# Kernel tuning notes

Hardware: AMD Instinct MI355X
Metric: run time of the kernel (lower is better)

## Reference

```python
import jax, jax.numpy as jnp
import numpy as np

N = 50000      # num_nodes
E = 800000     # num_edges (avg degree 16)
D = 128        # embedding_dim
HID = 32       # per-head hidden dim of conv1
H = 8          # heads of conv1
OUT = 128      # output_dim


def setup_inputs() -> dict:
    key = jax.random.key(0)
    ks = jax.random.split(key, 14)
    s = lambda fan_in: 1.0 / np.sqrt(fan_in)
    return {
        "x": jax.random.randint(ks[0], (N,), 0, N),
        "edge_index": jax.random.randint(ks[1], (2, E), 0, N),
        "emb": jax.random.normal(ks[2], (N, D), jnp.float32),
        # conv1: GATConv(D, HID, heads=H, concat=True)
        "W1": jax.random.normal(ks[3], (D, H * HID), jnp.float32) * s(D),
        "a_src1": jax.random.normal(ks[4], (H, HID), jnp.float32) * s(HID),
        "a_dst1": jax.random.normal(ks[5], (H, HID), jnp.float32) * s(HID),
        "b1": jnp.zeros((H * HID,), jnp.float32),
        # conv2: GATConv(H*HID, OUT, heads=1, concat=False)
        "W2": jax.random.normal(ks[6], (H * HID, OUT), jnp.float32) * s(H * HID),
        "a_src2": jax.random.normal(ks[7], (1, OUT), jnp.float32) * s(OUT),
        "a_dst2": jax.random.normal(ks[8], (1, OUT), jnp.float32) * s(OUT),
        "b2": jnp.zeros((OUT,), jnp.float32),
        # output Linear(OUT, OUT)
        "Wo": jax.random.normal(ks[9], (OUT, OUT), jnp.float32) * s(OUT),
        "bo": jnp.zeros((OUT,), jnp.float32),
    }


def _segment_softmax(e, seg, n):
    # e: [E, H]; softmax over edges sharing the same destination node
    m = jax.ops.segment_max(e, seg, num_segments=n)            # [N, H]
    ex = jnp.exp(e - m[seg])
    denom = jax.ops.segment_sum(ex, seg, num_segments=n)       # [N, H]
    return ex / (denom[seg] + 1e-16)


def _gat_conv(x, src, dst, W, a_src, a_dst, b, concat):
    n = x.shape[0]
    Hh, C = a_src.shape
    h = (x @ W).reshape(n, Hh, C)                              # [N, H, C]
    al_src = (h * a_src).sum(-1)                               # [N, H]
    al_dst = (h * a_dst).sum(-1)                               # [N, H]
    e = jax.nn.leaky_relu(al_src[src] + al_dst[dst], 0.2)      # [E, H]
    alpha = _segment_softmax(e, dst, n)                        # [E, H]
    out = jax.ops.segment_sum(h[src] * alpha[:, :, None], dst, num_segments=n)
    out = out.reshape(n, Hh * C) if concat else out.mean(axis=1)
    return out + b


def reference(x, edge_index, emb, W1, a_src1, a_dst1, b1,
              W2, a_src2, a_dst2, b2, Wo, bo):
    n = x.shape[0]
    loops = jnp.arange(n)
    src = jnp.concatenate([edge_index[0], loops])              # add self-loops (PyG default)
    dst = jnp.concatenate([edge_index[1], loops])
    h = emb[x]                                                 # [N, D]
    h = _gat_conv(h, src, dst, W1, a_src1, a_dst1, b1, concat=True)
    h = _gat_conv(h, src, dst, W2, a_src2, a_dst2, b2, concat=False)
    return h @ Wo + bo
```

## Files before the change

kernel.cpp:

```cpp
#include <hip/hip_runtime.h>
#include <hip/hip_bf16.h>

#define NN 50000
#define EE 800000
#define DD 128
#define F1 256
#define F2 128

using short8  = __attribute__((ext_vector_type(8))) short;
using floatx4 = __attribute__((ext_vector_type(4))) float;

__device__ inline float bf2f(ushort u) { return __uint_as_float(((unsigned)u) << 16); }
__device__ inline ushort f2bf(float f) {
    unsigned u = __float_as_uint(f);
    u += 0x7fffu + ((u >> 16) & 1u);
    return (ushort)(u >> 16);
}

#define HB ((EE + 255) / 256)
#define GB ((NN + 1) / 2)
#define W1B ((DD * F1 + 255) / 256)
#define W2B ((F1 * F2 + 255) / 256)

__global__ __launch_bounds__(256) void k_prep(
    const int* __restrict__ edst, int* __restrict__ cnt,
    const int* __restrict__ x, const float* __restrict__ emb, ushort* __restrict__ Ax,
    const float* __restrict__ W1, ushort* __restrict__ W1t,
    const float* __restrict__ W2, ushort* __restrict__ W2t,
    const float* __restrict__ Wo, ushort* __restrict__ Wot) {
    int b = blockIdx.x;
    if (b < HB) {
        int i = b * 256 + threadIdx.x;
        if (i < EE) atomicAdd(&cnt[edst[i]], 1);
    } else if (b < HB + GB) {
        int row = (b - HB) * 2 + (threadIdx.x >> 7);
        if (row < NN) {
            int c = threadIdx.x & 127;
            Ax[(size_t)row * DD + c] = f2bf(emb[(size_t)x[row] * DD + c]);
        }
    } else if (b < HB + GB + W1B) {
        int idx = (b - HB - GB) * 256 + threadIdx.x;
        int k = idx / F1, n = idx % F1;
        W1t[(size_t)n * DD + k] = f2bf(W1[(size_t)k * F1 + n]);
    } else if (b < HB + GB + W1B + W2B) {
        int idx = (b - HB - GB - W1B) * 256 + threadIdx.x;
        int k = idx / F2, n = idx % F2;
        W2t[(size_t)n * F1 + k] = f2bf(W2[(size_t)k * F2 + n]);
    } else {
        int idx = (b - HB - GB - W1B - W2B) * 256 + threadIdx.x;
        int k = idx / F2, n = idx % F2;
        Wot[(size_t)n * F2 + k] = f2bf(Wo[(size_t)k * F2 + n]);
    }
}

__global__ void k_scan1(const int* __restrict__ cnt, int* __restrict__ out,
                        int* __restrict__ sums) {
    __shared__ int s[256];
    int i = blockIdx.x * 256 + threadIdx.x;
    int v = (i < NN) ? cnt[i] + 1 : 0;
    s[threadIdx.x] = v;
    __syncthreads();
    for (int off = 1; off < 256; off <<= 1) {
        int t = (threadIdx.x >= off) ? s[threadIdx.x - off] : 0;
        __syncthreads();
        s[threadIdx.x] += t;
        __syncthreads();
    }
    if (i < NN) out[i] = s[threadIdx.x] - v;
    if (threadIdx.x == 255) sums[blockIdx.x] = s[255];
}

__global__ void k_scan2(int* __restrict__ sums, int nb) {
    __shared__ int s[256];
    int v = (threadIdx.x < nb) ? sums[threadIdx.x] : 0;
    s[threadIdx.x] = v;
    __syncthreads();
    for (int off = 1; off < 256; off <<= 1) {
        int t = (threadIdx.x >= off) ? s[threadIdx.x - off] : 0;
        __syncthreads();
        s[threadIdx.x] += t;
        __syncthreads();
    }
    if (threadIdx.x < nb) sums[threadIdx.x] = s[threadIdx.x] - v;
}

__global__ void k_scan3(int* __restrict__ offsets, const int* __restrict__ sums,
                        int* __restrict__ cursor) {
    int i = blockIdx.x * 256 + threadIdx.x;
    if (i < NN) {
        int v = offsets[i] + sums[blockIdx.x];
        offsets[i] = v;
        cursor[i] = v;
    }
    if (blockIdx.x == 0 && threadIdx.x == 0) offsets[NN] = EE + NN;
}

__global__ void k_scatter(const int* __restrict__ esrc, const int* __restrict__ edst,
                          int* __restrict__ cursor, int* __restrict__ srcs) {
    int i = blockIdx.x * 256 + threadIdx.x;
    if (i < EE) {
        int pos = atomicAdd(&cursor[edst[i]], 1);
        srcs[pos] = esrc[i];
    } else if (i < EE + NN) {
        int n = i - EE;
        int pos = atomicAdd(&cursor[n], 1);
        srcs[pos] = n;
    }
}

template<int K, bool FINAL>
__global__ __launch_bounds__(256, 2) void k_mfma_gemm(
    const ushort* __restrict__ A, const ushort* __restrict__ Bt,
    void* __restrict__ Cout, int ldc, const float* __restrict__ bias) {
    __shared__ ushort As[128][72];
    __shared__ ushort Bs[128][72];
    const int t    = threadIdx.x;
    const int lane = t & 63;
    const int w    = t >> 6;
    const int wr   = w >> 1, wc = w & 1;
    const int m0   = blockIdx.x * 128;
    const int n0   = blockIdx.y * 128;
    floatx4 acc[4][4] = {};
    for (int k0 = 0; k0 < K; k0 += 64) {
        #pragma unroll
        for (int p = 0; p < 4; ++p) {
            int linear = p * 2048 + t * 8;
            int row = linear >> 6;
            int col = linear & 63;
            short8 va = {};
            int gm = m0 + row;
            if (gm < NN) va = *(const short8*)(A + (size_t)gm * K + k0 + col);
            *(short8*)&As[row][col] = va;
            short8 vb = *(const short8*)(Bt + (size_t)(n0 + row) * K + k0 + col);
            *(short8*)&Bs[row][col] = vb;
        }
        __syncthreads();
        #pragma unroll
        for (int kk = 0; kk < 64; kk += 32) {
            const int q8 = (lane >> 4) * 8;
            short8 af[4], bf[4];
            #pragma unroll
            for (int i = 0; i < 4; ++i)
                af[i] = *(const short8*)&As[wr * 64 + i * 16 + (lane & 15)][kk + q8];
            #pragma unroll
            for (int j = 0; j < 4; ++j)
                bf[j] = *(const short8*)&Bs[wc * 64 + j * 16 + (lane & 15)][kk + q8];
            #pragma unroll
            for (int i = 0; i < 4; ++i)
                #pragma unroll
                for (int j = 0; j < 4; ++j)
                    acc[i][j] = __builtin_amdgcn_mfma_f32_16x16x32_bf16(
                        af[i], bf[j], acc[i][j], 0, 0, 0);
        }
        __syncthreads();
    }
    const int r0 = (lane >> 4) * 4;
    const int cc = lane & 15;
    #pragma unroll
    for (int i = 0; i < 4; ++i) {
        #pragma unroll
        for (int r = 0; r < 4; ++r) {
            int m = m0 + wr * 64 + i * 16 + r0 + r;
            if (m >= NN) continue;
            #pragma unroll
            for (int j = 0; j < 4; ++j) {
                int n = n0 + wc * 64 + j * 16 + cc;
                float v = acc[i][j][r];
                if (FINAL) ((float*)Cout)[(size_t)m * ldc + n] = v + bias[n];
                else       ((ushort*)Cout)[(size_t)m * ldc + n] = f2bf(v);
            }
        }
    }
}

__global__ __launch_bounds__(256) void k_al1(const ushort* __restrict__ h1,
                                             const float* __restrict__ a_src1,
                                             const float* __restrict__ a_dst1,
                                             float* __restrict__ a1s, float* __restrict__ a1d) {
    int n = blockIdx.x * 4 + (threadIdx.x >> 6);
    if (n >= NN) return;
    int lane = threadIdx.x & 63;
    ushort4 hu = *(const ushort4*)(h1 + (size_t)n * F1 + lane * 4);
    float4 hv = make_float4(bf2f(hu.x), bf2f(hu.y), bf2f(hu.z), bf2f(hu.w));
    float4 as  = *(const float4*)(a_src1 + lane * 4);
    float4 adv = *(const float4*)(a_dst1 + lane * 4);
    float ps = hv.x * as.x + hv.y * as.y + hv.z * as.z + hv.w * as.w;
    float pd = hv.x * adv.x + hv.y * adv.y + hv.z * adv.z + hv.w * adv.w;
    #pragma unroll
    for (int off = 1; off < 8; off <<= 1) {
        ps += __shfl_xor(ps, off);
        pd += __shfl_xor(pd, off);
    }
    if ((lane & 7) == 0) {
        a1s[n * 8 + (lane >> 3)] = ps;
        a1d[n * 8 + (lane >> 3)] = pd;
    }
}

__global__ __launch_bounds__(256) void k_al2(const ushort* __restrict__ h2,
                                             const float* __restrict__ a_src2,
                                             const float* __restrict__ a_dst2,
                                             float* __restrict__ a2s, float* __restrict__ a2d) {
    int n = blockIdx.x * 4 + (threadIdx.x >> 6);
    if (n >= NN) return;
    int lane = threadIdx.x & 63;
    ushort2 hu = *(const ushort2*)(h2 + (size_t)n * F2 + lane * 2);
    float2 hv = make_float2(bf2f(hu.x), bf2f(hu.y));
    float2 as  = *(const float2*)(a_src2 + lane * 2);
    float2 adv = *(const float2*)(a_dst2 + lane * 2);
    float ps = hv.x * as.x + hv.y * as.y;
    float pd = hv.x * adv.x + hv.y * adv.y;
    #pragma unroll
    for (int off = 1; off < 64; off <<= 1) {
        ps += __shfl_xor(ps, off);
        pd += __shfl_xor(pd, off);
    }
    if (lane == 0) { a2s[n] = ps; a2d[n] = pd; }
}

__device__ inline float lrelu(float x) { return x > 0.f ? x : 0.2f * x; }

__global__ __launch_bounds__(256) void k_agg1(
    const int* __restrict__ offsets, const int* __restrict__ srcs,
    const ushort* __restrict__ h1, const float* __restrict__ a1s,
    const float* __restrict__ a1d, const float* __restrict__ b1,
    ushort* __restrict__ out1) {
    __shared__ float atab[4][512];
    __shared__ int   stab[4][64];
    const int w = threadIdx.x >> 6;
    const int d = blockIdx.x * 4 + w;
    if (d >= NN) return;
    const int lane = threadIdx.x & 63;
    const int beg = offsets[d], end = offsets[d + 1];
    const int e8 = lane >> 3, h8 = lane & 7;
    const float ad = a1d[d * 8 + h8];
    float m = -1e30f, den = 0.f;
    for (int i = beg + e8; i < end; i += 8) {
        int s = srcs[i];
        float v = lrelu(a1s[s * 8 + h8] + ad);
        float nm = fmaxf(m, v);
        den = den * __expf(m - nm) + __expf(v - nm);
        m = nm;
    }
    #pragma unroll
    for (int mask = 8; mask < 64; mask <<= 1) {
        float om = __shfl_xor(m, mask);
        float od = __shfl_xor(den, mask);
        float nm = fmaxf(m, om);
        den = den * __expf(m - nm) + od * __expf(om - nm);
        m = nm;
    }
    float rden = 1.f / (den + 1e-16f);
    const int sl = ((lane & 7) << 3) | (lane >> 3);
    const float mh  = __shfl(m, sl);
    const float rdh = __shfl(rden, sl);
    float4 acc = make_float4(0.f, 0.f, 0.f, 0.f);
    const int hh = lane >> 3;
    for (int tb = beg; tb < end; tb += 64) {
        int cnt = min(64, end - tb);
        if (lane < cnt) stab[w][lane] = srcs[tb + lane];
        int np = cnt * 8;
        for (int p = lane; p < np; p += 64) {
            int s = stab[w][p >> 3];
            float v = lrelu(a1s[s * 8 + h8] + ad);
            atab[w][p] = __expf(v - m) * rden;
        }
        for (int e = 0; e < cnt; ++e) {
            int s = stab[w][e];
            float alpha = atab[w][e * 8 + hh];
            ushort4 u = *(const ushort4*)(h1 + (size_t)s * F1 + lane * 4);
            acc.x += alpha * bf2f(u.x); acc.y += alpha * bf2f(u.y);
            acc.z += alpha * bf2f(u.z); acc.w += alpha * bf2f(u.w);
        }
    }
    (void)mh; (void)rdh;
    float4 bb = *(const float4*)(b1 + lane * 4);
    ushort4 o;
    o.x = f2bf(acc.x + bb.x); o.y = f2bf(acc.y + bb.y);
    o.z = f2bf(acc.z + bb.z); o.w = f2bf(acc.w + bb.w);
    *(ushort4*)(out1 + (size_t)d * F1 + lane * 4) = o;
}

__global__ __launch_bounds__(256) void k_agg2(
    const int* __restrict__ offsets, const int* __restrict__ srcs,
    const ushort* __restrict__ h2, const float* __restrict__ a2s,
    const float* __restrict__ a2d, const float* __restrict__ b2,
    ushort* __restrict__ out2) {
    __shared__ float atab[4][64];
    __shared__ int   stab[4][64];
    const int w = threadIdx.x >> 6;
    const int d = blockIdx.x * 4 + w;
    if (d >= NN) return;
    const int lane = threadIdx.x & 63;
    const int beg = offsets[d], end = offsets[d + 1];
    const float ad = a2d[d];
    float m = -1e30f, den = 0.f;
    for (int i = beg + lane; i < end; i += 64) {
        int s = srcs[i];
        float v = lrelu(a2s[s] + ad);
        float nm = fmaxf(m, v);
        den = den * __expf(m - nm) + __expf(v - nm);
        m = nm;
    }
    #pragma unroll
    for (int mask = 1; mask < 64; mask <<= 1) {
        float om = __shfl_xor(m, mask);
        float od = __shfl_xor(den, mask);
        float nm = fmaxf(m, om);
        den = den * __expf(m - nm) + od * __expf(om - nm);
        m = nm;
    }
    float rden = 1.f / (den + 1e-16f);
    float2 acc = make_float2(0.f, 0.f);
    for (int tb = beg; tb < end; tb += 64) {
        int cnt = min(64, end - tb);
        if (lane < cnt) {
            int s = srcs[tb + lane];
            stab[w][lane] = s;
            atab[w][lane] = __expf(lrelu(a2s[s] + ad) - m) * rden;
        }
        for (int e = 0; e < cnt; ++e) {
            int s = stab[w][e];
            float alpha = atab[w][e];
            ushort2 u = *(const ushort2*)(h2 + (size_t)s * F2 + lane * 2);
            acc.x += alpha * bf2f(u.x); acc.y += alpha * bf2f(u.y);
        }
    }
    float2 bb = *(const float2*)(b2 + lane * 2);
    ushort2 o;
    o.x = f2bf(acc.x + bb.x); o.y = f2bf(acc.y + bb.y);
    *(ushort2*)(out2 + (size_t)d * F2 + lane * 2) = o;
}

extern "C" void kernel_launch(void* const* d_in, const int* in_sizes, int n_in,
                              void* d_out, int out_size, void* d_ws, size_t ws_size,
                              hipStream_t stream) {
    const int*   x      = (const int*)d_in[0];
    const int*   edge   = (const int*)d_in[1];
    const float* emb    = (const float*)d_in[2];
    const float* W1     = (const float*)d_in[3];
    const float* a_src1 = (const float*)d_in[4];
    const float* a_dst1 = (const float*)d_in[5];
    const float* b1     = (const float*)d_in[6];
    const float* W2     = (const float*)d_in[7];
    const float* a_src2 = (const float*)d_in[8];
    const float* a_dst2 = (const float*)d_in[9];
    const float* b2     = (const float*)d_in[10];
    const float* Wo     = (const float*)d_in[11];
    const float* bo     = (const float*)d_in[12];
    float* out = (float*)d_out;

    char* w = (char*)d_ws;
    auto alloc = [&](size_t bytes) {
        char* p = w;
        w += (bytes + 255) & ~(size_t)255;
        return p;
    };
    int*    offsets = (int*)alloc((NN + 1) * sizeof(int));
    int*    cursor  = (int*)alloc(NN * sizeof(int));
    int*    sums    = (int*)alloc(256 * sizeof(int));
    int*    srcs    = (int*)alloc((size_t)(EE + NN) * sizeof(int));
    ushort* Ax      = (ushort*)alloc((size_t)NN * DD * sizeof(ushort));
    ushort* W1t     = (ushort*)alloc((size_t)DD * F1 * sizeof(ushort));
    ushort* W2t     = (ushort*)alloc((size_t)F1 * F2 * sizeof(ushort));
    ushort* Wot     = (ushort*)alloc((size_t)F2 * F2 * sizeof(ushort));
    ushort* h1      = (ushort*)alloc((size_t)NN * F1 * sizeof(ushort));
    ushort* out1    = (ushort*)alloc((size_t)NN * F1 * sizeof(ushort));
    ushort* h2      = (ushort*)alloc((size_t)NN * F2 * sizeof(ushort));
    ushort* out2    = (ushort*)alloc((size_t)NN * F2 * sizeof(ushort));
    float*  a1s     = (float*)alloc((size_t)NN * 8 * sizeof(float));
    float*  a1d     = (float*)alloc((size_t)NN * 8 * sizeof(float));
    float*  a2s     = a1s;
    float*  a2d     = a1d;

    const int* esrc = edge;
    const int* edst = edge + EE;

    const int NB = (NN + 255) / 256;

    hipMemsetAsync(cursor, 0, NN * sizeof(int), stream);
    k_prep<<<HB + GB + W1B + W2B + ((F2 * F2 + 255) / 256), 256, 0, stream>>>(
        edst, cursor, x, emb, Ax, W1, W1t, W2, W2t, Wo, Wot);
    k_scan1<<<NB, 256, 0, stream>>>(cursor, offsets, sums);
    k_scan2<<<1, 256, 0, stream>>>(sums, NB);
    k_scan3<<<NB, 256, 0, stream>>>(offsets, sums, cursor);
    k_scatter<<<(EE + NN + 255) / 256, 256, 0, stream>>>(esrc, edst, cursor, srcs);

    const int MT = (NN + 127) / 128;

    k_mfma_gemm<DD, false><<<dim3(MT, F1 / 128), 256, 0, stream>>>(Ax, W1t, h1, F1, nullptr);
    k_al1<<<(NN + 3) / 4, 256, 0, stream>>>(h1, a_src1, a_dst1, a1s, a1d);
    k_agg1<<<(NN + 3) / 4, 256, 0, stream>>>(offsets, srcs, h1, a1s, a1d, b1, out1);

    k_mfma_gemm<F1, false><<<dim3(MT, 1), 256, 0, stream>>>(out1, W2t, h2, F2, nullptr);
    k_al2<<<(NN + 3) / 4, 256, 0, stream>>>(h2, a_src2, a_dst2, a2s, a2d);
    k_agg2<<<(NN + 3) / 4, 256, 0, stream>>>(offsets, srcs, h2, a2s, a2d, b2, out2);

    k_mfma_gemm<F2, true><<<dim3(MT, 1), 256, 0, stream>>>(out2, Wot, out, F2, bo);
}
```

Before: 378.4 us.

## Fuse attention logits into GEMM epilogues, merge scan kernels, unroll gather loops

Computes the per-head source and destination attention logits inside the MFMA GEMM epilogue from fp32 accumulators, using cross-lane shuffles and shared memory. This removes the separate k_al1 and k_al2 kernels that re-read h1 and h2 from memory. It also folds the single-block scan of block sums into the offset-add kernel, so every block redundantly rescans the sums, and unrolls the aggregation gather loops by four to put more loads in flight. The logits now come from unrounded fp32 values rather than the bf16-rounded h, which slightly changes numerics, and the epilogue adds shuffle and register work.

```diff
diff --git a/kernel.cpp b/kernel.cpp
--- a/kernel.cpp
+++ b/kernel.cpp
@@ -21,6 +21,7 @@
 #define GB ((NN + 1) / 2)
 #define W1B ((DD * F1 + 255) / 256)
 #define W2B ((F1 * F2 + 255) / 256)
+#define WOB ((F2 * F2 + 255) / 256)
 
 __global__ __launch_bounds__(256) void k_prep(
     const int* __restrict__ edst, int* __restrict__ cnt,
@@ -70,7 +71,8 @@
     if (threadIdx.x == 255) sums[blockIdx.x] = s[255];
 }
 
-__global__ void k_scan2(int* __restrict__ sums, int nb) {
+__global__ void k_scan3(int* __restrict__ offsets, const int* __restrict__ sums,
+                        int* __restrict__ cursor, int nb) {
     __shared__ int s[256];
     int v = (threadIdx.x < nb) ? sums[threadIdx.x] : 0;
     s[threadIdx.x] = v;
@@ -81,16 +83,12 @@
         s[threadIdx.x] += t;
         __syncthreads();
     }
-    if (threadIdx.x < nb) sums[threadIdx.x] = s[threadIdx.x] - v;
-}
-
-__global__ void k_scan3(int* __restrict__ offsets, const int* __restrict__ sums,
-                        int* __restrict__ cursor) {
+    int base = (blockIdx.x == 0) ? 0 : s[blockIdx.x - 1];
     int i = blockIdx.x * 256 + threadIdx.x;
     if (i < NN) {
-        int v = offsets[i] + sums[blockIdx.x];
-        offsets[i] = v;
-        cursor[i] = v;
+        int o = offsets[i] + base;
+        offsets[i] = o;
+        cursor[i] = o;
     }
     if (blockIdx.x == 0 && threadIdx.x == 0) offsets[NN] = EE + NN;
 }
@@ -108,12 +106,15 @@
     }
 }
 
-template<int K, bool FINAL>
+template<int K, int MODE>
 __global__ __launch_bounds__(256, 2) void k_mfma_gemm(
     const ushort* __restrict__ A, const ushort* __restrict__ Bt,
-    void* __restrict__ Cout, int ldc, const float* __restrict__ bias) {
+    void* __restrict__ Cout, int ldc, const float* __restrict__ bias,
+    const float* __restrict__ avs, const float* __restrict__ avd,
+    float* __restrict__ out_s, float* __restrict__ out_d) {
     __shared__ ushort As[128][72];
     __shared__ ushort Bs[128][72];
+    __shared__ float als[2][128], ald[2][128];
     const int t    = threadIdx.x;
     const int lane = t & 63;
     const int w    = t >> 6;
@@ -154,68 +155,76 @@
         }
         __syncthreads();
     }
-    const int r0 = (lane >> 4) * 4;
+    const int q  = lane >> 4;
+    const int r0 = q * 4;
     const int cc = lane & 15;
+    float as0, as1, as2, as3, ad0, ad1, ad2, ad3;
+    if (MODE == 1 || MODE == 2) {
+        as0 = avs[n0 + wc * 64 +  0 + cc]; ad0 = avd[n0 + wc * 64 +  0 + cc];
+        as1 = avs[n0 + wc * 64 + 16 + cc]; ad1 = avd[n0 + wc * 64 + 16 + cc];
+        as2 = avs[n0 + wc * 64 + 32 + cc]; ad2 = avd[n0 + wc * 64 + 32 + cc];
+        as3 = avs[n0 + wc * 64 + 48 + cc]; ad3 = avd[n0 + wc * 64 + 48 + cc];
+    }
     #pragma unroll
     for (int i = 0; i < 4; ++i) {
         #pragma unroll
         for (int r = 0; r < 4; ++r) {
             int m = m0 + wr * 64 + i * 16 + r0 + r;
-            if (m >= NN) continue;
-            #pragma unroll
-            for (int j = 0; j < 4; ++j) {
-                int n = n0 + wc * 64 + j * 16 + cc;
-                float v = acc[i][j][r];
-                if (FINAL) ((float*)Cout)[(size_t)m * ldc + n] = v + bias[n];
-                else       ((ushort*)Cout)[(size_t)m * ldc + n] = f2bf(v);
+            if (MODE == 1) {
+                float hs0 = acc[i][0][r] * as0 + acc[i][1][r] * as1;
+                float hs1 = acc[i][2][r] * as2 + acc[i][3][r] * as3;
+                float hd0 = acc[i][0][r] * ad0 + acc[i][1][r] * ad1;
+                float hd1 = acc[i][2][r] * ad2 + acc[i][3][r] * ad3;
+                #pragma unroll
+                for (int mask = 1; mask < 16; mask <<= 1) {
+                    hs0 += __shfl_xor(hs0, mask);
+                    hs1 += __shfl_xor(hs1, mask);
+                    hd0 += __shfl_xor(hd0, mask);
+                    hd1 += __shfl_xor(hd1, mask);
+                }
+                if (cc == 0 && m < NN) {
+                    int gh = (n0 >> 5) + wc * 2;
+                    out_s[m * 8 + gh] = hs0;   out_s[m * 8 + gh + 1] = hs1;
+                    out_d[m * 8 + gh] = hd0;   out_d[m * 8 + gh + 1] = hd1;
+                }
             }
-        }
-    }
-}
-
-__global__ __launch_bounds__(256) void k_al1(const ushort* __restrict__ h1,
-                                             const float* __restrict__ a_src1,
-                                             const float* __restrict__ a_dst1,
-                                             float* __restrict__ a1s, float* __restrict__ a1d) {
-    int n = blockIdx.x * 4 + (threadIdx.x >> 6);
-    if (n >= NN) return;
-    int lane = threadIdx.x & 63;
-    ushort4 hu = *(const ushort4*)(h1 + (size_t)n * F1 + lane * 4);
-    float4 hv = make_float4(bf2f(hu.x), bf2f(hu.y), bf2f(hu.z), bf2f(hu.w));
-    float4 as  = *(const float4*)(a_src1 + lane * 4);
-    float4 adv = *(const float4*)(a_dst1 + lane * 4);
-    float ps = hv.x * as.x + hv.y * as.y + hv.z * as.z + hv.w * as.w;
-    float pd = hv.x * adv.x + hv.y * adv.y + hv.z * adv.z + hv.w * adv.w;
-    #pragma unroll
-    for (int off = 1; off < 8; off <<= 1) {
-        ps += __shfl_xor(ps, off);
-        pd += __shfl_xor(pd, off);
-    }
-    if ((lane & 7) == 0) {
-        a1s[n * 8 + (lane >> 3)] = ps;
-        a1d[n * 8 + (lane >> 3)] = pd;
-    }
-}
-
-__global__ __launch_bounds__(256) void k_al2(const ushort* __restrict__ h2,
-                                             const float* __restrict__ a_src2,
-                                             const float* __restrict__ a_dst2,
-                                             float* __restrict__ a2s, float* __restrict__ a2d) {
-    int n = blockIdx.x * 4 + (threadIdx.x >> 6);
-    if (n >= NN) return;
-    int lane = threadIdx.x & 63;
-    ushort2 hu = *(const ushort2*)(h2 + (size_t)n * F2 + lane * 2);
-    float2 hv = make_float2(bf2f(hu.x), bf2f(hu.y));
-    float2 as  = *(const float2*)(a_src2 + lane * 2);
-    float2 adv = *(const float2*)(a_dst2 + lane * 2);
-    float ps = hv.x * as.x + hv.y * as.y;
-    float pd = hv.x * adv.x + hv.y * adv.y;
-    #pragma unroll
-    for (int off = 1; off < 64; off <<= 1) {
-        ps += __shfl_xor(ps, off);
-        pd += __shfl_xor(pd, off);
-    }
-    if (lane == 0) { a2s[n] = ps; a2d[n] = pd; }
+            if (MODE == 2) {
+                float ps = acc[i][0][r] * as0 + acc[i][1][r] * as1
+                         + acc[i][2][r] * as2 + acc[i][3][r] * as3;
+                float pd = acc[i][0][r] * ad0 + acc[i][1][r] * ad1
+                         + acc[i][2][r] * ad2 + acc[i][3][r] * ad3;
+                #pragma unroll
+                for (int mask = 1; mask < 16; mask <<= 1) {
+                    ps += __shfl_xor(ps, mask);
+                    pd += __shfl_xor(pd, mask);
+                }
+                if (cc == 0) {
+                    int lr = wr * 64 + i * 16 + r0 + r;
+                    als[wc][lr] = ps;
+                    ald[wc][lr] = pd;
+                }
+            }
+            if (m < NN) {
+                #pragma unroll
+                for (int j = 0; j < 4; ++j) {
+                    int n = n0 + wc * 64 + j * 16 + cc;
+                    float v = acc[i][j][r];
+                    if (MODE == 3) ((float*)Cout)[(size_t)m * ldc + n] = v + bias[n];
+                    else           ((ushort*)Cout)[(size_t)m * ldc + n] = f2bf(v);
+                }
+            }
+        }
+    }
+    if (MODE == 2) {
+        __syncthreads();
+        if (t < 128) {
+            int m = m0 + t;
+            if (m < NN) {
+                out_s[m] = als[0][t] + als[1][t];
+                out_d[m] = ald[0][t] + ald[1][t];
+            }
+        }
+    }
 }
 
 __device__ inline float lrelu(float x) { return x > 0.f ? x : 0.2f * x; }
@@ -251,9 +260,6 @@
         m = nm;
     }
     float rden = 1.f / (den + 1e-16f);
-    const int sl = ((lane & 7) << 3) | (lane >> 3);
-    const float mh  = __shfl(m, sl);
-    const float rdh = __shfl(rden, sl);
     float4 acc = make_float4(0.f, 0.f, 0.f, 0.f);
     const int hh = lane >> 3;
     for (int tb = beg; tb < end; tb += 64) {
@@ -265,7 +271,24 @@
             float v = lrelu(a1s[s * 8 + h8] + ad);
             atab[w][p] = __expf(v - m) * rden;
         }
-        for (int e = 0; e < cnt; ++e) {
+        int e = 0;
+        for (; e + 4 <= cnt; e += 4) {
+            int s0 = stab[w][e], s1 = stab[w][e + 1];
+            int s2 = stab[w][e + 2], s3 = stab[w][e + 3];
+            ushort4 u0 = *(const ushort4*)(h1 + (size_t)s0 * F1 + lane * 4);
+            ushort4 u1 = *(const ushort4*)(h1 + (size_t)s1 * F1 + lane * 4);
+            ushort4 u2 = *(const ushort4*)(h1 + (size_t)s2 * F1 + lane * 4);
+            ushort4 u3 = *(const ushort4*)(h1 + (size_t)s3 * F1 + lane * 4);
+            float a0 = atab[w][(e + 0) * 8 + hh];
+            float a1 = atab[w][(e + 1) * 8 + hh];
+            float a2 = atab[w][(e + 2) * 8 + hh];
+            float a3 = atab[w][(e + 3) * 8 + hh];
+            acc.x += a0 * bf2f(u0.x) + a1 * bf2f(u1.x) + a2 * bf2f(u2.x) + a3 * bf2f(u3.x);
+            acc.y += a0 * bf2f(u0.y) + a1 * bf2f(u1.y) + a2 * bf2f(u2.y) + a3 * bf2f(u3.y);
+            acc.z += a0 * bf2f(u0.z) + a1 * bf2f(u1.z) + a2 * bf2f(u2.z) + a3 * bf2f(u3.z);
+            acc.w += a0 * bf2f(u0.w) + a1 * bf2f(u1.w) + a2 * bf2f(u2.w) + a3 * bf2f(u3.w);
+        }
+        for (; e < cnt; ++e) {
             int s = stab[w][e];
             float alpha = atab[w][e * 8 + hh];
             ushort4 u = *(const ushort4*)(h1 + (size_t)s * F1 + lane * 4);
@@ -273,7 +296,6 @@
             acc.z += alpha * bf2f(u.z); acc.w += alpha * bf2f(u.w);
         }
     }
-    (void)mh; (void)rdh;
     float4 bb = *(const float4*)(b1 + lane * 4);
     ushort4 o;
     o.x = f2bf(acc.x + bb.x); o.y = f2bf(acc.y + bb.y);
@@ -319,7 +341,20 @@
             stab[w][lane] = s;
             atab[w][lane] = __expf(lrelu(a2s[s] + ad) - m) * rden;
         }
-        for (int e = 0; e < cnt; ++e) {
+        int e = 0;
+        for (; e + 4 <= cnt; e += 4) {
+            int s0 = stab[w][e], s1 = stab[w][e + 1];
+            int s2 = stab[w][e + 2], s3 = stab[w][e + 3];
+            ushort2 u0 = *(const ushort2*)(h2 + (size_t)s0 * F2 + lane * 2);
+            ushort2 u1 = *(const ushort2*)(h2 + (size_t)s1 * F2 + lane * 2);
+            ushort2 u2 = *(const ushort2*)(h2 + (size_t)s2 * F2 + lane * 2);
+            ushort2 u3 = *(const ushort2*)(h2 + (size_t)s3 * F2 + lane * 2);
+            float a0 = atab[w][e + 0], a1 = atab[w][e + 1];
+            float a2 = atab[w][e + 2], a3 = atab[w][e + 3];
+            acc.x += a0 * bf2f(u0.x) + a1 * bf2f(u1.x) + a2 * bf2f(u2.x) + a3 * bf2f(u3.x);
+            acc.y += a0 * bf2f(u0.y) + a1 * bf2f(u1.y) + a2 * bf2f(u2.y) + a3 * bf2f(u3.y);
+        }
+        for (; e < cnt; ++e) {
             int s = stab[w][e];
             float alpha = atab[w][e];
             ushort2 u = *(const ushort2*)(h2 + (size_t)s * F2 + lane * 2);
@@ -379,22 +414,22 @@
     const int NB = (NN + 255) / 256;
 
     hipMemsetAsync(cursor, 0, NN * sizeof(int), stream);
-    k_prep<<<HB + GB + W1B + W2B + ((F2 * F2 + 255) / 256), 256, 0, stream>>>(
+    k_prep<<<HB + GB + W1B + W2B + WOB, 256, 0, stream>>>(
         edst, cursor, x, emb, Ax, W1, W1t, W2, W2t, Wo, Wot);
     k_scan1<<<NB, 256, 0, stream>>>(cursor, offsets, sums);
-    k_scan2<<<1, 256, 0, stream>>>(sums, NB);
-    k_scan3<<<NB, 256, 0, stream>>>(offsets, sums, cursor);
+    k_scan3<<<NB, 256, 0, stream>>>(offsets, sums, cursor, NB);
     k_scatter<<<(EE + NN + 255) / 256, 256, 0, stream>>>(esrc, edst, cursor, srcs);
 
     const int MT = (NN + 127) / 128;
 
-    k_mfma_gemm<DD, false><<<dim3(MT, F1 / 128), 256, 0, stream>>>(Ax, W1t, h1, F1, nullptr);
-    k_al1<<<(NN + 3) / 4, 256, 0, stream>>>(h1, a_src1, a_dst1, a1s, a1d);
+    k_mfma_gemm<DD, 1><<<dim3(MT, F1 / 128), 256, 0, stream>>>(
+        Ax, W1t, h1, F1, nullptr, a_src1, a_dst1, a1s, a1d);
     k_agg1<<<(NN + 3) / 4, 256, 0, stream>>>(offsets, srcs, h1, a1s, a1d, b1, out1);
 
-    k_mfma_gemm<F1, false><<<dim3(MT, 1), 256, 0, stream>>>(out1, W2t, h2, F2, nullptr);
-    k_al2<<<(NN + 3) / 4, 256, 0, stream>>>(h2, a_src2, a_dst2, a2s, a2d);
+    k_mfma_gemm<F1, 2><<<dim3(MT, 1), 256, 0, stream>>>(
+        out1, W2t, h2, F2, nullptr, a_src2, a_dst2, a2s, a2d);
     k_agg2<<<(NN + 3) / 4, 256, 0, stream>>>(offsets, srcs, h2, a2s, a2d, b2, out2);
 
-    k_mfma_gemm<F2, true><<<dim3(MT, 1), 256, 0, stream>>>(out2, Wot, out, F2, bo);
-}
+    k_mfma_gemm<F2, 3><<<dim3(MT, 1), 256, 0, stream>>>(
+        out2, Wot, out, F2, bo, nullptr, nullptr, nullptr, nullptr);
+}
```

After: 366.4 us. 1.03x faster.
